# Optimization experiments

Hardware: AMD Instinct MI355X
Metric: run time of the kernel (lower is better)

## Reference

```python
import jax, jax.numpy as jnp
import numpy as np

ALPHA = 0.2  # LeakyReLU negative slope
NEG_INF = -9e15


def setup_inputs() -> dict:
    key = jax.random.key(0)
    ks = jax.random.split(key, 6)
    B, N, F_IN, F_OUT = 4, 1024, 64, 64
    h = jax.random.normal(ks[0], (B, N, F_IN), dtype=jnp.float32)
    adj = jax.random.randint(ks[1], (B, N, N), 0, 2, dtype=jnp.int32)
    lin_w = jax.random.normal(ks[2], (F_OUT, F_IN), dtype=jnp.float32) * (1.0 / np.sqrt(F_IN))
    lin_b = jax.random.normal(ks[3], (F_OUT,), dtype=jnp.float32) * 0.02
    W_w = jax.random.normal(ks[4], (F_OUT, 2 * F_OUT), dtype=jnp.float32) * (1.0 / np.sqrt(2 * F_OUT))
    a = jax.random.normal(ks[5], (F_OUT, 1), dtype=jnp.float32) * (1.414 / np.sqrt(F_OUT))
    return {"h": h, "adj": adj, "lin_w": lin_w, "lin_b": lin_b, "W_w": W_w, "a": a}


def reference(h, adj, lin_w, lin_b, W_w, a):
    F_OUT = lin_w.shape[0]
    # h' = Linear(h): (B, N, F_OUT)
    hp = jnp.einsum('bni,oi->bno', h, lin_w) + lin_b
    # W @ concat(h_i, h_j) == h_i @ W1^T + h_j @ W2^T  (same math, no 2F concat)
    W1, W2 = W_w[:, :F_OUT], W_w[:, F_OUT:]
    u = jnp.einsum('bnf,of->bno', hp, W1)  # source/row term   (B, N, F_OUT)
    v = jnp.einsum('bnf,of->bno', hp, W2)  # target/col term   (B, N, F_OUT)
    s = u[:, :, None, :] + v[:, None, :, :]        # (B, N, N, F_OUT)
    s = jnp.where(s > 0, s, ALPHA * s)             # LeakyReLU
    e = jnp.einsum('bijf,f->bij', s, a[:, 0])      # (B, N, N)
    e = jnp.where(adj > 0, e, NEG_INF)
    attention = jax.nn.softmax(e, axis=2)
    h_prime = jnp.einsum('bij,bjf->bif', attention, hp)
    return jax.nn.elu(h_prime)
```

## Files before the change

### kernel.cpp

```cpp
#include <hip/hip_runtime.h>
#include <hip/hip_bf16.h>
#include <math.h>

constexpr int B = 4;
constexpr int N = 1024;
constexpr float NEGINF = -9000000000000000.0f;

__global__ __launch_bounds__(256) void gat_prep(
    const float* __restrict__ h, const float* __restrict__ lin_w,
    const float* __restrict__ lin_b, const float* __restrict__ W_w,
    const float* __restrict__ a_g,
    float* __restrict__ hp, float* __restrict__ u_out, float* __restrict__ vT,
    float* __restrict__ au_out, float* __restrict__ av_out) {
  __shared__ float hs[64 * 18];
  __shared__ float wl[64 * 68];
  __shared__ float w1[64 * 68];
  __shared__ float w2[64 * 68];
  __shared__ float hpT[64 * 18];
  __shared__ float vt_s[64 * 17];
  __shared__ float ared[2][16 * 17];
  __shared__ float lb_s[64], a_s[64];

  const int b = blockIdx.x >> 6;
  const int n0 = (blockIdx.x & 63) << 4;
  const int tid = threadIdx.x;

  if (tid < 64) { lb_s[tid] = lin_b[tid]; a_s[tid] = a_g[tid]; }
  for (int idx = tid; idx < 1024; idx += 256) {
    const int r = idx >> 6, c = idx & 63;
    hs[c * 18 + r] = h[((b << 10) + n0 + r) * 64 + c];
  }
  for (int idx = tid; idx < 4096; idx += 256) {
    const int o = idx >> 6, f = idx & 63;
    wl[f * 68 + o] = lin_w[idx];
    w1[f * 68 + o] = W_w[o * 128 + f];
    w2[f * 68 + o] = W_w[o * 128 + 64 + f];
  }
  __syncthreads();

  const int tf = tid & 15, tn = tid >> 4;
  float ahp[4];
#pragma unroll
  for (int r = 0; r < 4; ++r) ahp[r] = lb_s[tf * 4 + r];
#pragma unroll 8
  for (int k = 0; k < 64; ++k) {
    const float hv = hs[k * 18 + tn];
    const float4 l4 = *(const float4*)&wl[k * 68 + tf * 4];
    ahp[0] = fmaf(hv, l4.x, ahp[0]);
    ahp[1] = fmaf(hv, l4.y, ahp[1]);
    ahp[2] = fmaf(hv, l4.z, ahp[2]);
    ahp[3] = fmaf(hv, l4.w, ahp[3]);
  }
  const int row = (b << 10) + n0 + tn;
  *(float4*)&hp[row * 64 + tf * 4] = make_float4(ahp[0], ahp[1], ahp[2], ahp[3]);
#pragma unroll
  for (int r = 0; r < 4; ++r) hpT[(tf * 4 + r) * 18 + tn] = ahp[r];
  __syncthreads();

  float aU[4] = {0.f, 0.f, 0.f, 0.f}, aV[4] = {0.f, 0.f, 0.f, 0.f};
#pragma unroll 8
  for (int k = 0; k < 64; ++k) {
    const float hv = hpT[k * 18 + tn];
    const float4 u4 = *(const float4*)&w1[k * 68 + tf * 4];
    const float4 v4 = *(const float4*)&w2[k * 68 + tf * 4];
    aU[0] = fmaf(hv, u4.x, aU[0]);
    aU[1] = fmaf(hv, u4.y, aU[1]);
    aU[2] = fmaf(hv, u4.z, aU[2]);
    aU[3] = fmaf(hv, u4.w, aU[3]);
    aV[0] = fmaf(hv, v4.x, aV[0]);
    aV[1] = fmaf(hv, v4.y, aV[1]);
    aV[2] = fmaf(hv, v4.z, aV[2]);
    aV[3] = fmaf(hv, v4.w, aV[3]);
  }
  *(float4*)&u_out[row * 64 + tf * 4] = make_float4(aU[0], aU[1], aU[2], aU[3]);
  float aup = 0.f, avp = 0.f;
#pragma unroll
  for (int r = 0; r < 4; ++r) {
    vt_s[(tf * 4 + r) * 17 + tn] = aV[r];
    aup = fmaf(a_s[tf * 4 + r], aU[r], aup);
    avp = fmaf(a_s[tf * 4 + r], aV[r], avp);
  }
  ared[0][tn * 17 + tf] = aup;
  ared[1][tn * 17 + tf] = avp;
  __syncthreads();
  for (int idx = tid; idx < 1024; idx += 256) {
    const int f = idx >> 4, n = idx & 15;
    vT[(((b << 6) + f) << 10) + n0 + n] = vt_s[f * 17 + n];
  }
  if (tid < 32) {
    const int which = tid >> 4, rr = tid & 15;
    float s2 = 0.f;
#pragma unroll
    for (int t = 0; t < 16; ++t) s2 += ared[which][rr * 17 + t];
    if (which == 0) au_out[(b << 10) + n0 + rr] = s2;
    else av_out[(b << 10) + n0 + rr] = s2;
  }
}

__global__ __launch_bounds__(256) void gat_attn(
    const float* __restrict__ u_g, const float* __restrict__ vT,
    const float* __restrict__ hp, const int* __restrict__ adj,
    const float* __restrict__ a_g, const float* __restrict__ au_g,
    const float* __restrict__ av_g, float* __restrict__ out) {
  __shared__ float p_s[4 * 1024];
  __shared__ float u_s[64 * 4];
  __shared__ float a_s[64];
  __shared__ float au_s[4];
  __shared__ float wred[4][4];
  __shared__ float wsum[4][4];
  __shared__ float rinv_s[4];

  const int b = blockIdx.x >> 8;
  const int i0 = (blockIdx.x & 255) << 2;
  const int tid = threadIdx.x;
  const int lane = tid & 63, w = tid >> 6;
  const int j0 = tid << 2;

  if (tid < 64) a_s[tid] = a_g[tid];
  if (tid < 4) au_s[tid] = au_g[(b << 10) + i0 + tid];
  {
    const int i = tid >> 6, f = tid & 63;
    u_s[f * 4 + i] = u_g[((b << 10) + i0 + i) * 64 + f];
  }

  const int* adjb = adj + (((b << 10) + i0) << 10) + j0;
  int4 ad4[4];
#pragma unroll
  for (int i = 0; i < 4; ++i) ad4[i] = *(const int4*)&adjb[i << 10];
  const float4 av4 = *(const float4*)&av_g[(b << 10) + j0];

  __syncthreads();

  float e[4][4];
#pragma unroll
  for (int i = 0; i < 4; ++i)
#pragma unroll
    for (int k = 0; k < 4; ++k) e[i][k] = 0.f;

  const float* vb = vT + ((b << 6) << 10);
#pragma unroll 8
  for (int f = 0; f < 64; ++f) {
    const float af = a_s[f];
    const float4 v4 = *(const float4*)&vb[(f << 10) + j0];
    const float4 u4 = *(const float4*)&u_s[f * 4];
    const float uu[4] = {u4.x, u4.y, u4.z, u4.w};
    const float vv[4] = {v4.x, v4.y, v4.z, v4.w};
#pragma unroll
    for (int i = 0; i < 4; ++i)
#pragma unroll
      for (int k = 0; k < 4; ++k)
        e[i][k] = fmaf(af, fabsf(uu[i] + vv[k]), e[i][k]);
  }
  const float avv[4] = {0.6f * av4.x, 0.6f * av4.y, 0.6f * av4.z, 0.6f * av4.w};
  float au6[4];
#pragma unroll
  for (int i = 0; i < 4; ++i) au6[i] = 0.6f * au_s[i];
#pragma unroll
  for (int i = 0; i < 4; ++i) {
    const int adv[4] = {ad4[i].x, ad4[i].y, ad4[i].z, ad4[i].w};
#pragma unroll
    for (int k = 0; k < 4; ++k) {
      const float ev = fmaf(0.4f, e[i][k], au6[i] + avv[k]);
      e[i][k] = adv[k] > 0 ? ev : NEGINF;
    }
  }

#pragma unroll
  for (int i = 0; i < 4; ++i) {
    float mm = fmaxf(fmaxf(e[i][0], e[i][1]), fmaxf(e[i][2], e[i][3]));
#pragma unroll
    for (int off = 32; off; off >>= 1) mm = fmaxf(mm, __shfl_xor(mm, off));
    if (lane == 0) wred[w][i] = mm;
  }
  __syncthreads();
#pragma unroll
  for (int i = 0; i < 4; ++i) {
    const float mi = fmaxf(fmaxf(wred[0][i], wred[1][i]),
                           fmaxf(wred[2][i], wred[3][i]));
#pragma unroll
    for (int k = 0; k < 4; ++k) e[i][k] = __expf(e[i][k] - mi);
    float ss = e[i][0] + e[i][1] + e[i][2] + e[i][3];
#pragma unroll
    for (int off = 32; off; off >>= 1) ss += __shfl_xor(ss, off);
    if (lane == 0) wsum[w][i] = ss;
  }
  __syncthreads();
  if (tid < 4)
    rinv_s[tid] = 1.0f / (wsum[0][tid] + wsum[1][tid] + wsum[2][tid] + wsum[3][tid]);
#pragma unroll
  for (int i = 0; i < 4; ++i)
    *(float4*)&p_s[(i << 10) + j0] = make_float4(e[i][0], e[i][1], e[i][2], e[i][3]);
  __syncthreads();

  const int fl = tid & 63, g = tid >> 6;
  float acc[4] = {0.f, 0.f, 0.f, 0.f};
  const float* hpb = hp + (b << 16);
#pragma unroll 4
  for (int jj = g << 8; jj < (g << 8) + 256; jj += 4) {
    const float4 p0 = *(const float4*)&p_s[jj];
    const float4 p1 = *(const float4*)&p_s[1024 + jj];
    const float4 p2 = *(const float4*)&p_s[2048 + jj];
    const float4 p3 = *(const float4*)&p_s[3072 + jj];
    float hv[4];
#pragma unroll
    for (int t = 0; t < 4; ++t) hv[t] = hpb[((jj + t) << 6) + fl];
    acc[0] += p0.x * hv[0] + p0.y * hv[1] + p0.z * hv[2] + p0.w * hv[3];
    acc[1] += p1.x * hv[0] + p1.y * hv[1] + p1.z * hv[2] + p1.w * hv[3];
    acc[2] += p2.x * hv[0] + p2.y * hv[1] + p2.z * hv[2] + p2.w * hv[3];
    acc[3] += p3.x * hv[0] + p3.y * hv[1] + p3.z * hv[2] + p3.w * hv[3];
  }
  __syncthreads();
  float* red = p_s;
#pragma unroll
  for (int i = 0; i < 4; ++i) red[(((g << 2) + i) << 6) + fl] = acc[i];
  __syncthreads();
  {
    const int i = tid >> 6, f = tid & 63;
    float r = red[((i) << 6) + f] + red[((4 + i) << 6) + f] +
              red[((8 + i) << 6) + f] + red[((12 + i) << 6) + f];
    r *= rinv_s[i];
    out[((b << 10) + i0 + i) * 64 + f] = r > 0.f ? r : expm1f(r);
  }
}

extern "C" void kernel_launch(void* const* d_in, const int* in_sizes, int n_in,
                              void* d_out, int out_size, void* d_ws, size_t ws_size,
                              hipStream_t stream) {
  const float* h = (const float*)d_in[0];
  const int* adj = (const int*)d_in[1];
  const float* lin_w = (const float*)d_in[2];
  const float* lin_b = (const float*)d_in[3];
  const float* W_w = (const float*)d_in[4];
  const float* a = (const float*)d_in[5];
  float* outp = (float*)d_out;

  float* ws = (float*)d_ws;
  float* hp = ws;
  float* u = ws + 262144;
  float* vT = ws + 524288;
  float* au = ws + 786432;
  float* av = ws + 790528;

  gat_prep<<<dim3(256), dim3(256), 0, stream>>>(h, lin_w, lin_b, W_w, a,
                                                hp, u, vT, au, av);
  gat_attn<<<dim3(1024), dim3(256), 0, stream>>>(u, vT, hp, adj, a, au, av, outp);
}
```

Measured before the change: 124.2 us.

## Register-tile attention-times-values with float4 hp loads and defer adjacency loads

The P·hp aggregation is restructured. Each thread now owns 4 rows by 4 features and reads hp as float4 over a 64-wide slice of j. The probabilities are stored transposed in shared memory so one float4 read gives all four rows for a column. A 16-way shared-memory reduction then combines the partial sums. Separately, the adjacency and av loads move from before the e-score loop to just before masking, and the unroll factor drops to 4, both to lower register pressure. The cost is that those global loads no longer overlap the score computation, plus a longer final reduction.

```diff
diff --git a/kernel.cpp b/kernel.cpp
--- a/kernel.cpp
+++ b/kernel.cpp
@@ -122,13 +122,6 @@
     const int i = tid >> 6, f = tid & 63;
     u_s[f * 4 + i] = u_g[((b << 10) + i0 + i) * 64 + f];
   }
-
-  const int* adjb = adj + (((b << 10) + i0) << 10) + j0;
-  int4 ad4[4];
-#pragma unroll
-  for (int i = 0; i < 4; ++i) ad4[i] = *(const int4*)&adjb[i << 10];
-  const float4 av4 = *(const float4*)&av_g[(b << 10) + j0];
-
   __syncthreads();
 
   float e[4][4];
@@ -137,11 +130,11 @@
 #pragma unroll
     for (int k = 0; k < 4; ++k) e[i][k] = 0.f;
 
-  const float* vb = vT + ((b << 6) << 10);
-#pragma unroll 8
+  const float* vb = vT + ((b << 6) << 10) + j0;
+#pragma unroll 4
   for (int f = 0; f < 64; ++f) {
     const float af = a_s[f];
-    const float4 v4 = *(const float4*)&vb[(f << 10) + j0];
+    const float4 v4 = *(const float4*)&vb[f << 10];
     const float4 u4 = *(const float4*)&u_s[f * 4];
     const float uu[4] = {u4.x, u4.y, u4.z, u4.w};
     const float vv[4] = {v4.x, v4.y, v4.z, v4.w};
@@ -151,13 +144,16 @@
       for (int k = 0; k < 4; ++k)
         e[i][k] = fmaf(af, fabsf(uu[i] + vv[k]), e[i][k]);
   }
+  const float4 av4 = *(const float4*)&av_g[(b << 10) + j0];
   const float avv[4] = {0.6f * av4.x, 0.6f * av4.y, 0.6f * av4.z, 0.6f * av4.w};
   float au6[4];
 #pragma unroll
   for (int i = 0; i < 4; ++i) au6[i] = 0.6f * au_s[i];
+  const int* adjb = adj + (((b << 10) + i0) << 10) + j0;
 #pragma unroll
   for (int i = 0; i < 4; ++i) {
-    const int adv[4] = {ad4[i].x, ad4[i].y, ad4[i].z, ad4[i].w};
+    const int4 ad = *(const int4*)&adjb[i << 10];
+    const int adv[4] = {ad.x, ad.y, ad.z, ad.w};
 #pragma unroll
     for (int k = 0; k < 4; ++k) {
       const float ev = fmaf(0.4f, e[i][k], au6[i] + avv[k]);
@@ -187,37 +183,50 @@
   __syncthreads();
   if (tid < 4)
     rinv_s[tid] = 1.0f / (wsum[0][tid] + wsum[1][tid] + wsum[2][tid] + wsum[3][tid]);
+
+#pragma unroll
+  for (int k = 0; k < 4; ++k)
+    *(float4*)&p_s[(tid << 2) + (k << 10)] =
+        make_float4(e[0][k], e[1][k], e[2][k], e[3][k]);
+  __syncthreads();
+
+  const int fq = tid & 15, g = tid >> 4;
+  float4 acc[4];
+#pragma unroll
+  for (int i = 0; i < 4; ++i) acc[i] = make_float4(0.f, 0.f, 0.f, 0.f);
+  const float* hpb = hp + (b << 16) + (fq << 2);
+#pragma unroll 4
+  for (int jj = 0; jj < 64; ++jj) {
+    const int j = (g << 6) + jj;
+    const float4 h4 = *(const float4*)&hpb[j << 6];
+    const float4 p4 = *(const float4*)&p_s[(j & ~3) + ((j & 3) << 10)];
+    acc[0].x = fmaf(p4.x, h4.x, acc[0].x);
+    acc[0].y = fmaf(p4.x, h4.y, acc[0].y);
+    acc[0].z = fmaf(p4.x, h4.z, acc[0].z);
+    acc[0].w = fmaf(p4.x, h4.w, acc[0].w);
+    acc[1].x = fmaf(p4.y, h4.x, acc[1].x);
+    acc[1].y = fmaf(p4.y, h4.y, acc[1].y);
+    acc[1].z = fmaf(p4.y, h4.z, acc[1].z);
+    acc[1].w = fmaf(p4.y, h4.w, acc[1].w);
+    acc[2].x = fmaf(p4.z, h4.x, acc[2].x);
+    acc[2].y = fmaf(p4.z, h4.y, acc[2].y);
+    acc[2].z = fmaf(p4.z, h4.z, acc[2].z);
+    acc[2].w = fmaf(p4.z, h4.w, acc[2].w);
+    acc[3].x = fmaf(p4.w, h4.x, acc[3].x);
+    acc[3].y = fmaf(p4.w, h4.y, acc[3].y);
+    acc[3].z = fmaf(p4.w, h4.z, acc[3].z);
+    acc[3].w = fmaf(p4.w, h4.w, acc[3].w);
+  }
+  __syncthreads();
 #pragma unroll
   for (int i = 0; i < 4; ++i)
-    *(float4*)&p_s[(i << 10) + j0] = make_float4(e[i][0], e[i][1], e[i][2], e[i][3]);
-  __syncthreads();
-
-  const int fl = tid & 63, g = tid >> 6;
-  float acc[4] = {0.f, 0.f, 0.f, 0.f};
-  const float* hpb = hp + (b << 16);
-#pragma unroll 4
-  for (int jj = g << 8; jj < (g << 8) + 256; jj += 4) {
-    const float4 p0 = *(const float4*)&p_s[jj];
-    const float4 p1 = *(const float4*)&p_s[1024 + jj];
-    const float4 p2 = *(const float4*)&p_s[2048 + jj];
-    const float4 p3 = *(const float4*)&p_s[3072 + jj];
-    float hv[4];
-#pragma unroll
-    for (int t = 0; t < 4; ++t) hv[t] = hpb[((jj + t) << 6) + fl];
-    acc[0] += p0.x * hv[0] + p0.y * hv[1] + p0.z * hv[2] + p0.w * hv[3];
-    acc[1] += p1.x * hv[0] + p1.y * hv[1] + p1.z * hv[2] + p1.w * hv[3];
-    acc[2] += p2.x * hv[0] + p2.y * hv[1] + p2.z * hv[2] + p2.w * hv[3];
-    acc[3] += p3.x * hv[0] + p3.y * hv[1] + p3.z * hv[2] + p3.w * hv[3];
-  }
-  __syncthreads();
-  float* red = p_s;
-#pragma unroll
-  for (int i = 0; i < 4; ++i) red[(((g << 2) + i) << 6) + fl] = acc[i];
+    *(float4*)&p_s[(g << 8) + (i << 6) + (fq << 2)] = acc[i];
   __syncthreads();
   {
     const int i = tid >> 6, f = tid & 63;
-    float r = red[((i) << 6) + f] + red[((4 + i) << 6) + f] +
-              red[((8 + i) << 6) + f] + red[((12 + i) << 6) + f];
+    float r = 0.f;
+#pragma unroll
+    for (int gg = 0; gg < 16; ++gg) r += p_s[(gg << 8) + (i << 6) + f];
     r *= rinv_s[i];
     out[((b << 10) + i0 + i) * 64 + f] = r > 0.f ? r : expm1f(r);
   }
```

After: 111.5 us. 1.11x faster.
